# Performance work log

Hardware: AMD Instinct MI355X
Metric: run time of the kernel (lower is better)

Reference implementation:

```python
import jax, jax.numpy as jnp
import numpy as np

B = 512     # graphs
NPG = 128   # nodes per graph
EPG = 2048  # edges per graph (avg degree 16)
IN = 128
HID = 128
K = 64      # ceil(0.5 * 128), SAGPooling ratio=0.5


def setup_inputs() -> dict:
    key = jax.random.key(0)
    ks = jax.random.split(key, 8)
    n_total = B * NPG
    x = jax.random.normal(ks[0], (n_total, IN), dtype=jnp.float32)
    # intra-graph random edges (PyG batching: edges never cross graphs)
    g = jnp.repeat(jnp.arange(B, dtype=jnp.int32), EPG)
    src = g * NPG + jax.random.randint(ks[1], (B * EPG,), 0, NPG, dtype=jnp.int32)
    dst = g * NPG + jax.random.randint(ks[2], (B * EPG,), 0, NPG, dtype=jnp.int32)
    edge_index = jnp.stack([src, dst], axis=0)
    batch = jnp.repeat(jnp.arange(B, dtype=jnp.int32), NPG)
    # params (glorot-ish scaling)
    W1 = jax.random.normal(ks[3], (IN, HID), dtype=jnp.float32) / np.sqrt(IN)
    b1 = jnp.zeros((HID,), dtype=jnp.float32)
    Ws = jax.random.normal(ks[4], (HID, 1), dtype=jnp.float32) / np.sqrt(HID)
    bs = jnp.zeros((1,), dtype=jnp.float32)
    Wlin = jax.random.normal(ks[5], (HID, HID), dtype=jnp.float32) / np.sqrt(HID)
    blin = jnp.zeros((HID,), dtype=jnp.float32)
    return {"x": x, "edge_index": edge_index, "batch": batch,
            "W1": W1, "b1": b1, "Ws": Ws, "bs": bs, "Wlin": Wlin, "blin": blin}


def _gcn_conv(x, src, dst, W, b, n):
    # PyG GCNConv: add self loops, symmetric deg^-1/2 norm, aggregate src->dst
    h = x @ W  # [n, out]
    loop = jnp.arange(n, dtype=src.dtype)
    s = jnp.concatenate([src, loop])
    d = jnp.concatenate([dst, loop])
    deg = jax.ops.segment_sum(jnp.ones(d.shape[0], dtype=x.dtype), d, num_segments=n)
    norm = jax.lax.rsqrt(deg)[s] * jax.lax.rsqrt(deg)[d]  # deg >= 1 via self loops
    msg = h[s] * norm[:, None]
    return jax.ops.segment_sum(msg, d, num_segments=n) + b


def reference(x, edge_index, batch, W1, b1, Ws, bs, Wlin, blin):
    n = x.shape[0]
    src, dst = edge_index[0], edge_index[1]
    # conv1 + relu
    h = jax.nn.relu(_gcn_conv(x, src, dst, W1, b1, n))  # [n, HID]
    # SAGPooling: score via GCNConv(HID -> 1)
    score = _gcn_conv(h, src, dst, Ws, bs, n)[:, 0]  # [n]
    # per-graph top-k on raw score (graphs are uniform NPG nodes -> dense top_k)
    score2 = score.reshape(B, NPG)
    top_v, top_i = jax.lax.top_k(score2, K)  # [B, K]
    h3 = h.reshape(B, NPG, HID)
    h_kept = jnp.take_along_axis(h3, top_i[:, :, None], axis=1)  # [B, K, HID]
    h_kept = h_kept * jnp.tanh(top_v)[:, :, None]  # x[perm] * tanh(score[perm])
    # global_mean_pool over kept nodes of each graph
    pooled = h_kept.mean(axis=1)  # [B, HID]
    return pooled @ Wlin + blin
```

## Files before the change

### kernel.cpp

```cpp
#include <hip/hip_runtime.h>
#include <math.h>

#define NPG  128
#define HID  128
#define KSEL 64
#define NT   256
#define HS   132
#define AS   17

typedef __attribute__((ext_vector_type(8))) __bf16 bfrag;
typedef __attribute__((ext_vector_type(4))) float f4;

static __device__ __forceinline__ __bf16 us2bf(unsigned short u) {
    union { unsigned short s; __bf16 b; } x; x.s = u; return x.b;
}
static __device__ __forceinline__ unsigned short bf2us(__bf16 b) {
    union { unsigned short s; __bf16 b; } x; x.b = b; return x.s;
}

__global__ __launch_bounds__(64) void wsplit_kernel(const float* __restrict__ W1,
                                                    bfrag* __restrict__ whi,
                                                    bfrag* __restrict__ wlo)
{
    const int b = blockIdx.x;
    const int ks = b >> 3, ct = b & 7;
    const int lane = threadIdx.x;
    const int n = lane & 15, quad = lane >> 4;
    bfrag h, l;
#pragma unroll
    for (int j = 0; j < 8; ++j) {
        const int k = ks * 32 + quad * 8 + j;
        float w = W1[k * HID + ct * 16 + n];
        __bf16 hh = (__bf16)w;
        h[j] = hh;
        l[j] = (__bf16)(w - (float)hh);
    }
    whi[b * 64 + lane] = h;
    wlo[b * 64 + lane] = l;
}

__global__ __launch_bounds__(NT, 2) void sagpool_fused(
    const float* __restrict__ x,
    const int*   __restrict__ esrc,
    const int*   __restrict__ edst,
    const bfrag* __restrict__ whi,
    const bfrag* __restrict__ wlo,
    const float* __restrict__ b1,
    const float* __restrict__ Ws,
    const float* __restrict__ bsp,
    const float* __restrict__ Wlin,
    const float* __restrict__ blin,
    float* __restrict__ out,
    int epg)
{
    __shared__ __align__(16) unsigned HpT[HID * HS];
    __shared__ __align__(16) unsigned AdjN[NPG * AS];
    __shared__ __align__(16) int   degl[NPG];
    __shared__ __align__(16) float rsl[NPG];
    __shared__ __align__(16) float spl[NPG];
    __shared__ __align__(16) float scl[NPG];
    __shared__ __align__(16) float wgt[NPG];
    __shared__ __align__(16) float pp[4 * HID];

    const int g = blockIdx.x, t = threadIdx.x;
    const int node0 = g * NPG;
    const long e0 = (long)g * epg;
    const int lane = t & 63, wv = t >> 6;
    const int n16 = lane & 15, quad = lane >> 4;
    const int m0 = wv * 32;

    int es[8], ed[8];
#pragma unroll
    for (int i = 0; i < 8; ++i) {
        int e = i * NT + t;
        es[i] = esrc[e0 + e] - node0;
        ed[i] = edst[e0 + e] - node0;
    }
    bfrag ah[8], al[8];
    {
        const float* xw = x + (long)(node0 + m0) * HID;
#pragma unroll
        for (int rt = 0; rt < 2; ++rt)
#pragma unroll
            for (int ks = 0; ks < 4; ++ks) {
                const float* xr = xw + (rt * 16 + n16) * HID + ks * 32 + quad * 8;
                float4 a = *reinterpret_cast<const float4*>(xr);
                float4 b = *reinterpret_cast<const float4*>(xr + 4);
                float vv[8] = {a.x, a.y, a.z, a.w, b.x, b.y, b.z, b.w};
                const int r = rt * 4 + ks;
#pragma unroll
                for (int j = 0; j < 8; ++j) {
                    __bf16 hb = (__bf16)vv[j];
                    ah[r][j] = hb;
                    al[r][j] = (__bf16)(vv[j] - (float)hb);
                }
            }
    }
    float b1v[8], wsv[8];
#pragma unroll
    for (int ct = 0; ct < 8; ++ct) {
        b1v[ct] = b1[ct * 16 + n16];
        wsv[ct] = Ws[ct * 16 + n16];
    }
    const float bsv = bsp[0];

    for (int i = t; i < NPG * AS; i += NT) AdjN[i] = 0u;
    if (t < NPG) degl[t] = 0;
    __syncthreads();

#pragma unroll
    for (int i = 0; i < 8; ++i) {
        atomicAdd(&AdjN[ed[i] * AS + (es[i] >> 3)], 1u << ((es[i] & 7) * 4));
        atomicAdd(&degl[ed[i]], 1);
    }

    f4 acc[2][8];
#pragma unroll
    for (int rt = 0; rt < 2; ++rt)
#pragma unroll
        for (int ct = 0; ct < 8; ++ct) {
            acc[rt][ct].x = 0.f; acc[rt][ct].y = 0.f;
            acc[rt][ct].z = 0.f; acc[rt][ct].w = 0.f;
        }
#pragma unroll
    for (int ks = 0; ks < 4; ++ks)
#pragma unroll
        for (int ct = 0; ct < 8; ++ct) {
            bfrag bh = whi[(ks * 8 + ct) * 64 + lane];
            bfrag bl = wlo[(ks * 8 + ct) * 64 + lane];
#pragma unroll
            for (int rt = 0; rt < 2; ++rt) {
                const int r = rt * 4 + ks;
                acc[rt][ct] = __builtin_amdgcn_mfma_f32_16x16x32_bf16(ah[r], bh, acc[rt][ct], 0, 0, 0);
                acc[rt][ct] = __builtin_amdgcn_mfma_f32_16x16x32_bf16(al[r], bh, acc[rt][ct], 0, 0, 0);
                acc[rt][ct] = __builtin_amdgcn_mfma_f32_16x16x32_bf16(ah[r], bl, acc[rt][ct], 0, 0, 0);
                acc[rt][ct] = __builtin_amdgcn_mfma_f32_16x16x32_bf16(al[r], bl, acc[rt][ct], 0, 0, 0);
            }
        }
    __syncthreads();

    if (t < NPG) {
        rsl[t] = rsqrtf((float)(degl[t] + 1));
        AdjN[t * AS + (t >> 3)] += 1u << ((t & 7) * 4);
    }
    __syncthreads();

#pragma unroll
    for (int rt = 0; rt < 2; ++rt) {
        const int mb = m0 + rt * 16 + quad * 4;
        f4 rs4 = *reinterpret_cast<const f4*>(&rsl[mb]);
#pragma unroll
        for (int ct = 0; ct < 8; ++ct) {
            uint4 st;
            unsigned pw[4];
#pragma unroll
            for (int reg = 0; reg < 4; ++reg) {
                float v = acc[rt][ct][reg] * rs4[reg];
                __bf16 hb = (__bf16)v;
                __bf16 lb = (__bf16)(v - (float)hb);
                pw[reg] = ((unsigned)bf2us(hb) << 16) | (unsigned)bf2us(lb);
            }
            st.x = pw[0]; st.y = pw[1]; st.z = pw[2]; st.w = pw[3];
            *reinterpret_cast<uint4*>(&HpT[(ct * 16 + n16) * HS + mb]) = st;
        }
    }
    __syncthreads();

    f4 hacc[2][8];
#pragma unroll
    for (int mt = 0; mt < 2; ++mt)
#pragma unroll
        for (int ct = 0; ct < 8; ++ct) {
            hacc[mt][ct].x = 0.f; hacc[mt][ct].y = 0.f;
            hacc[mt][ct].z = 0.f; hacc[mt][ct].w = 0.f;
        }
#pragma unroll
    for (int ks = 0; ks < 4; ++ks) {
        bfrag af[2];
#pragma unroll
        for (int mt = 0; mt < 2; ++mt) {
            unsigned w = AdjN[(m0 + mt * 16 + n16) * AS + ks * 4 + quad];
#pragma unroll
            for (int j = 0; j < 8; ++j)
                af[mt][j] = (__bf16)(float)((w >> (4 * j)) & 15u);
        }
#pragma unroll
        for (int ct = 0; ct < 8; ++ct) {
            const unsigned* bp = &HpT[(ct * 16 + n16) * HS + ks * 32 + quad * 8];
            uint4 w0 = *reinterpret_cast<const uint4*>(bp);
            uint4 w1 = *reinterpret_cast<const uint4*>(bp + 4);
            unsigned ww[8] = {w0.x, w0.y, w0.z, w0.w, w1.x, w1.y, w1.z, w1.w};
            bfrag bh, bl;
#pragma unroll
            for (int j = 0; j < 8; ++j) {
                bh[j] = us2bf((unsigned short)(ww[j] >> 16));
                bl[j] = us2bf((unsigned short)(ww[j] & 0xFFFFu));
            }
#pragma unroll
            for (int mt = 0; mt < 2; ++mt) {
                hacc[mt][ct] = __builtin_amdgcn_mfma_f32_16x16x32_bf16(af[mt], bh, hacc[mt][ct], 0, 0, 0);
                hacc[mt][ct] = __builtin_amdgcn_mfma_f32_16x16x32_bf16(af[mt], bl, hacc[mt][ct], 0, 0, 0);
            }
        }
    }

    f4 rsm[2];
#pragma unroll
    for (int mt = 0; mt < 2; ++mt)
        rsm[mt] = *reinterpret_cast<const f4*>(&rsl[m0 + mt * 16 + quad * 4]);
#pragma unroll
    for (int mt = 0; mt < 2; ++mt)
#pragma unroll
        for (int ct = 0; ct < 8; ++ct)
#pragma unroll
            for (int reg = 0; reg < 4; ++reg)
                hacc[mt][ct][reg] = fmaxf(hacc[mt][ct][reg] * rsm[mt][reg] + b1v[ct], 0.f);

    {
        float dot[2][4];
#pragma unroll
        for (int mt = 0; mt < 2; ++mt)
#pragma unroll
            for (int reg = 0; reg < 4; ++reg) dot[mt][reg] = 0.f;
#pragma unroll
        for (int ct = 0; ct < 8; ++ct)
#pragma unroll
            for (int mt = 0; mt < 2; ++mt)
#pragma unroll
                for (int reg = 0; reg < 4; ++reg)
                    dot[mt][reg] += hacc[mt][ct][reg] * wsv[ct];
#pragma unroll
        for (int d = 1; d < 16; d <<= 1)
#pragma unroll
            for (int mt = 0; mt < 2; ++mt)
#pragma unroll
                for (int reg = 0; reg < 4; ++reg)
                    dot[mt][reg] += __shfl_xor(dot[mt][reg], d, 64);
        if (n16 == 0) {
#pragma unroll
            for (int mt = 0; mt < 2; ++mt)
#pragma unroll
                for (int reg = 0; reg < 4; ++reg)
                    spl[m0 + mt * 16 + quad * 4 + reg] = rsm[mt][reg] * dot[mt][reg];
        }
    }
    __syncthreads();

    {
        float4* WL4 = reinterpret_cast<float4*>(HpT);
        const float4* Wg4 = reinterpret_cast<const float4*>(Wlin);
#pragma unroll
        for (int i = 0; i < 16; ++i)
            WL4[i * NT + t] = Wg4[i * NT + t];
    }

    if (t < NPG) {
        const unsigned* row = &AdjN[t * AS];
        float sc = 0.f;
#pragma unroll
        for (int w = 0; w < 16; ++w) {
            unsigned u = row[w];
            const float* sp = &spl[w * 8];
            sc += (float)(u & 15u)         * sp[0] + (float)((u >> 4)  & 15u) * sp[1]
                + (float)((u >> 8)  & 15u) * sp[2] + (float)((u >> 12) & 15u) * sp[3]
                + (float)((u >> 16) & 15u) * sp[4] + (float)((u >> 20) & 15u) * sp[5]
                + (float)((u >> 24) & 15u) * sp[6] + (float)(u >> 28)         * sp[7];
        }
        scl[t] = rsl[t] * sc + bsv;
    }
    __syncthreads();

    if (t < NPG) {
        float v = scl[t];
        int rank = 0;
#pragma unroll
        for (int j4 = 0; j4 < 32; ++j4) {
            float4 u = *reinterpret_cast<const float4*>(&scl[j4 * 4]);
            const int jb = j4 * 4;
            rank += (u.x > v || (u.x == v && jb     < t)) ? 1 : 0;
            rank += (u.y > v || (u.y == v && jb + 1 < t)) ? 1 : 0;
            rank += (u.z > v || (u.z == v && jb + 2 < t)) ? 1 : 0;
            rank += (u.w > v || (u.w == v && jb + 3 < t)) ? 1 : 0;
        }
        wgt[t] = (rank < KSEL) ? tanhf(v) * (1.0f / KSEL) : 0.f;
    }
    __syncthreads();

    {
        float p[8];
        f4 wm[2];
#pragma unroll
        for (int mt = 0; mt < 2; ++mt)
            wm[mt] = *reinterpret_cast<const f4*>(&wgt[m0 + mt * 16 + quad * 4]);
#pragma unroll
        for (int ct = 0; ct < 8; ++ct) {
            float s = 0.f;
#pragma unroll
            for (int mt = 0; mt < 2; ++mt)
#pragma unroll
                for (int reg = 0; reg < 4; ++reg)
                    s += wm[mt][reg] * hacc[mt][ct][reg];
            p[ct] = s;
        }
#pragma unroll
        for (int d = 16; d < 64; d <<= 1)
#pragma unroll
            for (int ct = 0; ct < 8; ++ct)
                p[ct] += __shfl_xor(p[ct], d, 64);
        if (quad == 0) {
#pragma unroll
            for (int ct = 0; ct < 8; ++ct)
                pp[wv * HID + ct * 16 + n16] = p[ct];
        }
    }
    __syncthreads();
    if (t < NPG)
        scl[t] = pp[t] + pp[HID + t] + pp[2 * HID + t] + pp[3 * HID + t];
    __syncthreads();

    {
        const int c = t & 127, hf = t >> 7;
        const float* WL = reinterpret_cast<const float*>(HpT);
        float s = 0.f;
#pragma unroll
        for (int k = hf * 64; k < hf * 64 + 64; ++k)
            s += scl[k] * WL[k * HID + c];
        pp[t] = s;
    }
    __syncthreads();
    if (t < NPG)
        out[(long)g * HID + t] = pp[t] + pp[t + 128] + blin[t];
}

extern "C" void kernel_launch(void* const* d_in, const int* in_sizes, int n_in,
                              void* d_out, int out_size, void* d_ws, size_t ws_size,
                              hipStream_t stream) {
    const float* x    = (const float*)d_in[0];
    const int*   ei   = (const int*)  d_in[1];
    const float* W1   = (const float*)d_in[3];
    const float* b1   = (const float*)d_in[4];
    const float* Ws   = (const float*)d_in[5];
    const float* bs   = (const float*)d_in[6];
    const float* Wlin = (const float*)d_in[7];
    const float* blin = (const float*)d_in[8];
    float* out = (float*)d_out;

    const int E = in_sizes[1] / 2;
    const int nnodes = in_sizes[0] / HID;
    const int B = nnodes / NPG;
    const int epg = E / B;

    bfrag* whi = reinterpret_cast<bfrag*>(d_ws);
    bfrag* wlo = whi + 32 * 64;

    wsplit_kernel<<<32, 64, 0, stream>>>(W1, whi, wlo);
    sagpool_fused<<<B, NT, 0, stream>>>(x, ei, ei + E, whi, wlo, b1, Ws, bs,
                                        Wlin, blin, out, epg);
}
```

Baseline: 113.1 us.

## Fuse W1 bf16 split into main kernel via LDS and derive degrees from adjacency nibbles

Removes the separate wsplit kernel launch. Each block now loads W1, splits it into hi/lo bf16 pairs and stores them packed in the shared HpT buffer in MFMA fragment order before the GEMM. The degree atomics are dropped: each node's degree comes from popcount-style nibble sums over its packed adjacency row, and one barrier is removed. Wlin is now read directly from global memory instead of being staged through LDS. In exchange every block redoes the W1 conversion and the final matvec makes global loads.

Result: no change. 111.7 us (median of 2 runs) (-1.3%).

```diff
diff --git a/kernel.cpp b/kernel.cpp
--- a/kernel.cpp
+++ b/kernel.cpp
@@ -7,6 +7,7 @@
 #define NT   256
 #define HS   132
 #define AS   17
+#define FS   516
 
 typedef __attribute__((ext_vector_type(8))) __bf16 bfrag;
 typedef __attribute__((ext_vector_type(4))) float f4;
@@ -18,33 +19,11 @@
     union { unsigned short s; __bf16 b; } x; x.b = b; return x.s;
 }
 
-__global__ __launch_bounds__(64) void wsplit_kernel(const float* __restrict__ W1,
-                                                    bfrag* __restrict__ whi,
-                                                    bfrag* __restrict__ wlo)
-{
-    const int b = blockIdx.x;
-    const int ks = b >> 3, ct = b & 7;
-    const int lane = threadIdx.x;
-    const int n = lane & 15, quad = lane >> 4;
-    bfrag h, l;
-#pragma unroll
-    for (int j = 0; j < 8; ++j) {
-        const int k = ks * 32 + quad * 8 + j;
-        float w = W1[k * HID + ct * 16 + n];
-        __bf16 hh = (__bf16)w;
-        h[j] = hh;
-        l[j] = (__bf16)(w - (float)hh);
-    }
-    whi[b * 64 + lane] = h;
-    wlo[b * 64 + lane] = l;
-}
-
 __global__ __launch_bounds__(NT, 2) void sagpool_fused(
     const float* __restrict__ x,
     const int*   __restrict__ esrc,
     const int*   __restrict__ edst,
-    const bfrag* __restrict__ whi,
-    const bfrag* __restrict__ wlo,
+    const float* __restrict__ W1,
     const float* __restrict__ b1,
     const float* __restrict__ Ws,
     const float* __restrict__ bsp,
@@ -55,7 +34,6 @@
 {
     __shared__ __align__(16) unsigned HpT[HID * HS];
     __shared__ __align__(16) unsigned AdjN[NPG * AS];
-    __shared__ __align__(16) int   degl[NPG];
     __shared__ __align__(16) float rsl[NPG];
     __shared__ __align__(16) float spl[NPG];
     __shared__ __align__(16) float scl[NPG];
@@ -105,13 +83,45 @@
     const float bsv = bsp[0];
 
     for (int i = t; i < NPG * AS; i += NT) AdjN[i] = 0u;
-    if (t < NPG) degl[t] = 0;
-    __syncthreads();
-
-#pragma unroll
-    for (int i = 0; i < 8; ++i) {
+    __syncthreads();
+
+    {
+        const float4* W4 = reinterpret_cast<const float4*>(W1);
+#pragma unroll
+        for (int i = 0; i < 16; ++i) {
+            const int fd = i * 256 + t;
+            float4 w = W4[fd];
+            const int dw = fd * 4;
+            const int k = dw >> 7, n = dw & 127;
+            const int p = (k >> 5) * 8 + (n >> 4);
+            const int lane0 = ((k >> 3) & 3) * 16 + (n & 15);
+            const int j = k & 7;
+            unsigned* base = &HpT[p * FS + lane0 * 8 + j];
+            float vv[4] = {w.x, w.y, w.z, w.w};
+#pragma unroll
+            for (int e = 0; e < 4; ++e) {
+                __bf16 hb = (__bf16)vv[e];
+                __bf16 lb = (__bf16)(vv[e] - (float)hb);
+                base[e * 8] = ((unsigned)bf2us(hb) << 16) | (unsigned)bf2us(lb);
+            }
+        }
+    }
+#pragma unroll
+    for (int i = 0; i < 8; ++i)
         atomicAdd(&AdjN[ed[i] * AS + (es[i] >> 3)], 1u << ((es[i] & 7) * 4));
-        atomicAdd(&degl[ed[i]], 1);
+    __syncthreads();
+
+    if (t < NPG) {
+        unsigned* row = &AdjN[t * AS];
+        unsigned sum = 0;
+#pragma unroll
+        for (int w = 0; w < 16; ++w) {
+            unsigned u = row[w];
+            unsigned b = (u & 0x0F0F0F0Fu) + ((u >> 4) & 0x0F0F0F0Fu);
+            sum += (b * 0x01010101u) >> 24;
+        }
+        rsl[t] = rsqrtf((float)(sum + 1));
+        row[t >> 3] += 1u << ((t & 7) * 4);
     }
 
     f4 acc[2][8];
@@ -126,8 +136,16 @@
     for (int ks = 0; ks < 4; ++ks)
 #pragma unroll
         for (int ct = 0; ct < 8; ++ct) {
-            bfrag bh = whi[(ks * 8 + ct) * 64 + lane];
-            bfrag bl = wlo[(ks * 8 + ct) * 64 + lane];
+            const unsigned* fp = &HpT[(ks * 8 + ct) * FS + lane * 8];
+            uint4 a0 = *reinterpret_cast<const uint4*>(fp);
+            uint4 a1 = *reinterpret_cast<const uint4*>(fp + 4);
+            unsigned ww[8] = {a0.x, a0.y, a0.z, a0.w, a1.x, a1.y, a1.z, a1.w};
+            bfrag bh, bl;
+#pragma unroll
+            for (int j = 0; j < 8; ++j) {
+                bh[j] = us2bf((unsigned short)(ww[j] >> 16));
+                bl[j] = us2bf((unsigned short)(ww[j] & 0xFFFFu));
+            }
 #pragma unroll
             for (int rt = 0; rt < 2; ++rt) {
                 const int r = rt * 4 + ks;
@@ -139,12 +157,6 @@
         }
     __syncthreads();
 
-    if (t < NPG) {
-        rsl[t] = rsqrtf((float)(degl[t] + 1));
-        AdjN[t * AS + (t >> 3)] += 1u << ((t & 7) * 4);
-    }
-    __syncthreads();
-
 #pragma unroll
     for (int rt = 0; rt < 2; ++rt) {
         const int mb = m0 + rt * 16 + quad * 4;
@@ -245,14 +257,6 @@
         }
     }
     __syncthreads();
-
-    {
-        float4* WL4 = reinterpret_cast<float4*>(HpT);
-        const float4* Wg4 = reinterpret_cast<const float4*>(Wlin);
-#pragma unroll
-        for (int i = 0; i < 16; ++i)
-            WL4[i * NT + t] = Wg4[i * NT + t];
-    }
 
     if (t < NPG) {
         const unsigned* row = &AdjN[t * AS];
@@ -320,11 +324,10 @@
 
     {
         const int c = t & 127, hf = t >> 7;
-        const float* WL = reinterpret_cast<const float*>(HpT);
         float s = 0.f;
-#pragma unroll
+#pragma unroll 8
         for (int k = hf * 64; k < hf * 64 + 64; ++k)
-            s += scl[k] * WL[k * HID + c];
+            s += scl[k] * Wlin[k * HID + c];
         pp[t] = s;
     }
     __syncthreads();
@@ -350,10 +353,6 @@
     const int B = nnodes / NPG;
     const int epg = E / B;
 
-    bfrag* whi = reinterpret_cast<bfrag*>(d_ws);
-    bfrag* wlo = whi + 32 * 64;
-
-    wsplit_kernel<<<32, 64, 0, stream>>>(W1, whi, wlo);
-    sagpool_fused<<<B, NT, 0, stream>>>(x, ei, ei + E, whi, wlo, b1, Ws, bs,
+    sagpool_fused<<<B, NT, 0, stream>>>(x, ei, ei + E, W1, b1, Ws, bs,
                                         Wlin, blin, out, epg);
 }
```
